# Kernel tuning notes

Hardware: AMD Instinct MI355X
Metric: run time of the kernel (lower is better)

The kernel has to match this reference:

```python
import jax, jax.numpy as jnp
import numpy as np
import math

B, S, E, H = 2, 2048, 768, 12
D = E // H            # head_dim = 64
FFN = 3072            # GeGLU hidden
WIN = 64              # local window size
GLOBAL_IDS = np.array([0])
EPS = 1e-5


def _rope(x):
    # x: [B,H,S,D]; interleaved rotary embedding, theta=10000 (lucidrains RotaryEmbedding)
    d = x.shape[-1]
    s = x.shape[-2]
    inv_freq = 1.0 / (10000.0 ** (jnp.arange(0, d, 2, dtype=jnp.float32) / d))
    freqs = jnp.arange(s, dtype=jnp.float32)[:, None] * inv_freq[None, :]  # [S, D/2]
    freqs = jnp.repeat(freqs, 2, axis=-1)                                   # [S, D]
    cos, sin = jnp.cos(freqs), jnp.sin(freqs)
    xp = x.reshape(x.shape[:-1] + (d // 2, 2))
    x_rot = jnp.stack([-xp[..., 1], xp[..., 0]], axis=-1).reshape(x.shape)
    return x * cos + x_rot * sin


def _layernorm(x, scale, bias):
    mu = jnp.mean(x, axis=-1, keepdims=True)
    var = jnp.mean(jnp.square(x - mu), axis=-1, keepdims=True)
    return (x - mu) * jax.lax.rsqrt(var + EPS) * scale + bias


def setup_inputs() -> dict:
    key = jax.random.key(0)
    ks = jax.random.split(key, 10)
    def xav(k, shape, gain):
        fan_out, fan_in = shape
        std = gain * math.sqrt(2.0 / (fan_in + fan_out))
        return jax.random.normal(k, shape, jnp.float32) * std
    g2 = math.sqrt(2.0)
    g13 = math.sqrt(1.0 / 3.0)
    return {
        "x": jax.random.normal(ks[0], (B, S, E), jnp.float32),
        "rel_pos_bias": jax.random.normal(ks[1], (B, S, S), jnp.float32),
        "mask": jnp.ones((B, S), dtype=bool),
        "wq_w": xav(ks[2], (E, E), g2), "wq_b": jnp.zeros((E,), jnp.float32),
        "wk_w": xav(ks[3], (E, E), g2), "wk_b": jnp.zeros((E,), jnp.float32),
        "wv_w": xav(ks[4], (E, E), g2), "wv_b": jnp.zeros((E,), jnp.float32),
        "fc_w": xav(ks[5], (E, E), g2), "fc_b": jnp.zeros((E,), jnp.float32),
        "pos_coeff": jnp.full((H, 1, 1), 0.01, jnp.float32),
        "gate_w": xav(ks[6], (FFN, E), g13), "gate_b": jnp.zeros((FFN,), jnp.float32),
        "value_w": xav(ks[7], (FFN, E), g2), "value_b": jnp.zeros((FFN,), jnp.float32),
        "down_w": xav(ks[8], (E, FFN), g2), "down_b": jnp.zeros((E,), jnp.float32),
        "ln1_s": jnp.ones((E,), jnp.float32), "ln1_b": jnp.zeros((E,), jnp.float32),
        "ln2_s": jnp.ones((E,), jnp.float32), "ln2_b": jnp.zeros((E,), jnp.float32),
    }


def _sparse_allow(mask):
    # static local-window + global-token pattern, [S,S] bool
    idx = jnp.arange(S)
    allow = jnp.abs(idx[:, None] - idx[None, :]) <= WIN
    gidx = jnp.asarray(GLOBAL_IDS)
    allow = allow.at[gidx, :].set(True)
    allow = allow.at[:, gidx].set(True)
    # combine with padding mask [B,S] broadcast over query rows
    return allow[None, None, :, :] & mask[:, None, None, :]  # [B,1,S,S]


def reference(x, rel_pos_bias, mask, wq_w, wq_b, wk_w, wk_b, wv_w, wv_b,
              fc_w, fc_b, pos_coeff, gate_w, gate_b, value_w, value_b,
              down_w, down_b, ln1_s, ln1_b, ln2_s, ln2_b):
    def heads(t):  # [B,S,E] -> [B,H,S,D]
        return t.reshape(B, S, H, D).transpose(0, 2, 1, 3)

    Q = _rope(heads(x @ wq_w.T + wq_b))
    K = _rope(heads(x @ wk_w.T + wk_b))
    V = heads(x @ wv_w.T + wv_b)

    scores = jnp.einsum('bhqd,bhkd->bhqk', Q, K) / math.sqrt(D)
    scores = scores + pos_coeff[None] * rel_pos_bias[:, None]     # [B,H,S,S]
    allow = _sparse_allow(mask)
    scores = jnp.where(allow, scores, -1e30)
    scores = scores - jnp.max(scores, axis=-1, keepdims=True)
    attn = jax.nn.softmax(scores, axis=-1)
    ctx = jnp.einsum('bhqk,bhkd->bhqd', attn, V)
    ctx = ctx.transpose(0, 2, 1, 3).reshape(B, S, E)
    attn_out = ctx @ fc_w.T + fc_b

    h = _layernorm(x + attn_out, ln1_s, ln1_b)
    gate = jax.nn.gelu(h @ gate_w.T + gate_b, approximate=False)
    ffn = (gate * (h @ value_w.T + value_b)) @ down_w.T + down_b
    return _layernorm(h + ffn, ln2_s, ln2_b)
```

## Files before the change

### kernel.cpp

```cpp
#include <hip/hip_runtime.h>
#include <math.h>

#define B_   2
#define S_   2048
#define E_   768
#define H_   12
#define D_   64
#define FFN_ 3072
#define WIN_ 64
#define MTOT (B_*S_)

typedef unsigned short ushort_t;
typedef unsigned short ushort8 __attribute__((ext_vector_type(8)));
typedef __bf16 bf16x8 __attribute__((ext_vector_type(8)));
typedef float f32x4 __attribute__((ext_vector_type(4)));
typedef _Float16 half_t;

__device__ __forceinline__ float b2f(ushort_t u) {
    union { unsigned int i; float f; } c; c.i = ((unsigned int)u) << 16; return c.f;
}
__device__ __forceinline__ ushort_t f2b(float f) {
    union { float f; unsigned int i; } c; c.f = f;
    unsigned int u = c.i;
    return (ushort_t)((u + 0x7fffu + ((u >> 16) & 1u)) >> 16);
}
__device__ __forceinline__ float gelu_f(float g) {
    return 0.5f * g * (1.f + erff(g * 0.70710678118654752440f));
}

typedef const __attribute__((address_space(1))) void* gptr_t;
typedef __attribute__((address_space(3))) void* lptr_t;
__device__ __forceinline__ void gload16(const void* g, void* l) {
    __builtin_amdgcn_global_load_lds((gptr_t)g,
        (lptr_t)(unsigned int)(unsigned long long)l, 16, 0, 0);
}

__device__ __forceinline__ void cvt8(const float* __restrict__ in,
                                     ushort_t* __restrict__ out, int idx)
{
    const float4* p = (const float4*)(in + (size_t)idx * 8);
    const float4 a = p[0], b = p[1];
    ushort8 o;
    o[0]=f2b(a.x); o[1]=f2b(a.y); o[2]=f2b(a.z); o[3]=f2b(a.w);
    o[4]=f2b(b.x); o[5]=f2b(b.y); o[6]=f2b(b.z); o[7]=f2b(b.w);
    *(ushort8*)(out + (size_t)idx*8) = o;
}

__global__ __launch_bounds__(256)
void prep_fused(const float* __restrict__ x,
                const float* __restrict__ wq_w, const float* __restrict__ wk_w,
                const float* __restrict__ wv_w, const float* __restrict__ fc_w,
                ushort_t* __restrict__ Xb, ushort_t* __restrict__ wqb,
                ushort_t* __restrict__ wkb, ushort_t* __restrict__ wvb,
                ushort_t* __restrict__ fcb, float2* __restrict__ ctab)
{
    const int id = blockIdx.x, tid = threadIdx.x;
    if (id < 1536) {
        cvt8(x, Xb, id*256 + tid);
    } else if (id < 1824) {
        cvt8(wq_w, wqb, (id-1536)*256 + tid);
    } else if (id < 2112) {
        cvt8(wk_w, wkb, (id-1824)*256 + tid);
    } else if (id < 2400) {
        cvt8(wv_w, wvb, (id-2112)*256 + tid);
    } else if (id < 2688) {
        cvt8(fc_w, fcb, (id-2400)*256 + tid);
    } else {
        const int idx = (id-2688)*256 + tid;
        const int s = idx >> 5, i = idx & 31;
        const float inv = exp2f(-(float)i * (13.287712379549449f/32.0f));
        const float fr = (float)s * inv;
        ctab[idx] = make_float2(cosf(fr), sinf(fr));
    }
}

template<int EPI, int BN>
__global__ __launch_bounds__(256)
void gemm_mfma(const ushort_t* __restrict__ A,
               const ushort_t* W0, const float* b0, void* C0,
               const ushort_t* W1, const float* b1, void* C1,
               const ushort_t* W2, const float* b2, void* C2,
               const void* __restrict__ aux, int M, int N, int K)
{
    constexpr int NWC = BN/64, NWR = 4/NWC, WROWS = 128/NWR, MF = WROWS/16;
    const ushort_t* W = W0; const float* bias = b0; void* C = C0;
    if (blockIdx.z == 1) { W = W1; bias = b1; C = C1; }
    else if (blockIdx.z == 2) { W = W2; bias = b2; C = C2; }

    __shared__ __align__(16) ushort_t As[128*32];
    __shared__ __align__(16) ushort_t Bs[BN*32];

    const int tid = threadIdx.x, wv = tid>>6, lane = tid&63;
    const int m0 = blockIdx.y*128, n0 = blockIdx.x*BN;
    const int wr = wv / NWC, wc = wv % NWC;
    const int lr16 = lane & 15, lkb = (lane>>4)<<3;

    f32x4 acc[MF][4];
#pragma unroll
    for (int i=0;i<MF;++i)
#pragma unroll
        for (int j=0;j<4;++j) acc[i][j] = f32x4{0.f,0.f,0.f,0.f};

    const char* Ab = (const char*)(A + (size_t)m0*K);
    const char* Wb = (const char*)(W + (size_t)n0*K);
    const size_t rb = (size_t)K*2;
    const int wbase = wv*1024, lby = lane*16;

    for (int kt = 0; kt < K; kt += 32) {
        const size_t kb = (size_t)kt*2;
        int n_ = wbase + lby;
        gload16(Ab + (size_t)(n_>>6)*rb + kb + (n_&63), (char*)As + wbase);
        n_ += 4096;
        gload16(Ab + (size_t)(n_>>6)*rb + kb + (n_&63), (char*)As + wbase + 4096);
        n_ = wbase + lby;
        gload16(Wb + (size_t)(n_>>6)*rb + kb + (n_&63), (char*)Bs + wbase);
        if (BN == 128) {
            n_ += 4096;
            gload16(Wb + (size_t)(n_>>6)*rb + kb + (n_&63), (char*)Bs + wbase + 4096);
        }
        __syncthreads();
        bf16x8 af[MF], bfr[4];
#pragma unroll
        for (int mf=0; mf<MF; ++mf)
            af[mf] = *(const bf16x8*)&As[(wr*WROWS + mf*16 + lr16)*32 + lkb];
#pragma unroll
        for (int nf=0; nf<4; ++nf)
            bfr[nf] = *(const bf16x8*)&Bs[(wc*64 + nf*16 + lr16)*32 + lkb];
#pragma unroll
        for (int mf=0; mf<MF; ++mf)
#pragma unroll
            for (int nf=0; nf<4; ++nf)
                acc[mf][nf] = __builtin_amdgcn_mfma_f32_16x16x32_bf16(af[mf], bfr[nf], acc[mf][nf], 0,0,0);
        __syncthreads();
    }

    const int colb = n0 + wc*64 + lr16;
    const int rowb = m0 + wr*WROWS + ((lane>>4)<<2);
#pragma unroll
    for (int nf=0; nf<4; ++nf) {
        const int col = colb + nf*16;
        const float bsv = bias[col];
#pragma unroll
        for (int mf=0; mf<MF; ++mf) {
            const int row = rowb + mf*16;
            const f32x4 a = acc[mf][nf];
#pragma unroll
            for (int r=0; r<4; ++r) {
                const size_t off = (size_t)(row+r)*N + col;
                const float v = a[r] + bsv;
                if constexpr (EPI == 0) {
                    ((ushort_t*)C)[off] = f2b(v);
                } else {
                    ((float*)C)[off] = v + ((const float*)aux)[off];
                }
            }
        }
    }
}

__global__ __launch_bounds__(256, 4)
void gemm_qkv(const ushort_t* __restrict__ A,
              const ushort_t* __restrict__ Wqkv,
              const float* __restrict__ bq, const float* __restrict__ bk,
              const float* __restrict__ bv,
              const float2* __restrict__ ctab,
              ushort_t* __restrict__ Qb, ushort_t* __restrict__ Kb,
              ushort_t* __restrict__ Vt)
{
    constexpr int NT   = 24;
    constexpr int ABY  = 128*64;
    constexpr int BUFB = 2*ABY;
    __shared__ __align__(16) char lds[2*BUFB];

    const int id  = blockIdx.x;
    const int xcd = id & 7, w = id >> 3;
    const int gy  = (xcd & 3)*8 + (w & 7);
    const int gx  = (xcd >> 2)*9 + (w >> 3);
    const int m0 = gy*128, n0 = gx*128;

    const int tid = threadIdx.x, wv = tid>>6, l = tid&63;
    const int wr = wv>>1, wc = wv&1;
    const int lr16 = l & 15;
    const int ck = (((l>>4) ^ ((lr16>>1)&3)) << 4);

    const int lr4   = l >> 2;
    const int sslot = ((l & 3) ^ ((l >> 3) & 3)) << 4;
    const char* Agp = (const char*)A    + (size_t)(m0 + wv*32 + lr4)*1536 + sslot;
    const char* Bgp = (const char*)Wqkv + (size_t)(n0 + wv*32 + lr4)*1536 + sslot;

    const int rA0 = (wr*64 +  0 + lr16)*64, rA1 = (wr*64 + 16 + lr16)*64;
    const int rA2 = (wr*64 + 32 + lr16)*64, rA3 = (wr*64 + 48 + lr16)*64;
    const int rB0 = ABY + (wc*64 +  0 + lr16)*64, rB1 = ABY + (wc*64 + 16 + lr16)*64;
    const int rB2 = ABY + (wc*64 + 32 + lr16)*64, rB3 = ABY + (wc*64 + 48 + lr16)*64;

    f32x4 acc[4][4];
#pragma unroll
    for (int i=0;i<4;++i)
#pragma unroll
        for (int j=0;j<4;++j) acc[i][j] = f32x4{0.f,0.f,0.f,0.f};

#define STGQ(tt, cb) { \
    char* dA = lds + (cb)*BUFB + wv*2048; \
    char* dB = lds + (cb)*BUFB + ABY + wv*2048; \
    const size_t ko = (size_t)(tt)*64; \
    gload16(Agp + ko,           dA); \
    gload16(Agp + ko + 16*1536, dA + 1024); \
    gload16(Bgp + ko,           dB); \
    gload16(Bgp + ko + 16*1536, dB + 1024); }

    STGQ(0, 0);
    __syncthreads();

    int c = 0;
#pragma unroll 1
    for (int t = 0; t < NT; ++t) {
        if (t < NT-1) STGQ(t+1, c^1);
        const char* Lb = lds + c*BUFB;
        const bf16x8 a0 = *(const bf16x8*)(Lb + rA0 + ck);
        const bf16x8 a1 = *(const bf16x8*)(Lb + rA1 + ck);
        const bf16x8 a2 = *(const bf16x8*)(Lb + rA2 + ck);
        const bf16x8 a3 = *(const bf16x8*)(Lb + rA3 + ck);
        const bf16x8 b0 = *(const bf16x8*)(Lb + rB0 + ck);
        const bf16x8 b1 = *(const bf16x8*)(Lb + rB1 + ck);
        const bf16x8 b2 = *(const bf16x8*)(Lb + rB2 + ck);
        const bf16x8 b3 = *(const bf16x8*)(Lb + rB3 + ck);
        __builtin_amdgcn_s_setprio(1);
        acc[0][0] = __builtin_amdgcn_mfma_f32_16x16x32_bf16(a0, b0, acc[0][0], 0,0,0);
        acc[1][0] = __builtin_amdgcn_mfma_f32_16x16x32_bf16(a1, b0, acc[1][0], 0,0,0);
        acc[2][0] = __builtin_amdgcn_mfma_f32_16x16x32_bf16(a2, b0, acc[2][0], 0,0,0);
        acc[3][0] = __builtin_amdgcn_mfma_f32_16x16x32_bf16(a3, b0, acc[3][0], 0,0,0);
        acc[0][1] = __builtin_amdgcn_mfma_f32_16x16x32_bf16(a0, b1, acc[0][1], 0,0,0);
        acc[1][1] = __builtin_amdgcn_mfma_f32_16x16x32_bf16(a1, b1, acc[1][1], 0,0,0);
        acc[2][1] = __builtin_amdgcn_mfma_f32_16x16x32_bf16(a2, b1, acc[2][1], 0,0,0);
        acc[3][1] = __builtin_amdgcn_mfma_f32_16x16x32_bf16(a3, b1, acc[3][1], 0,0,0);
        acc[0][2] = __builtin_amdgcn_mfma_f32_16x16x32_bf16(a0, b2, acc[0][2], 0,0,0);
        acc[1][2] = __builtin_amdgcn_mfma_f32_16x16x32_bf16(a1, b2, acc[1][2], 0,0,0);
        acc[2][2] = __builtin_amdgcn_mfma_f32_16x16x32_bf16(a2, b2, acc[2][2], 0,0,0);
        acc[3][2] = __builtin_amdgcn_mfma_f32_16x16x32_bf16(a3, b2, acc[3][2], 0,0,0);
        acc[0][3] = __builtin_amdgcn_mfma_f32_16x16x32_bf16(a0, b3, acc[0][3], 0,0,0);
        acc[1][3] = __builtin_amdgcn_mfma_f32_16x16x32_bf16(a1, b3, acc[1][3], 0,0,0);
        acc[2][3] = __builtin_amdgcn_mfma_f32_16x16x32_bf16(a2, b3, acc[2][3], 0,0,0);
        acc[3][3] = __builtin_amdgcn_mfma_f32_16x16x32_bf16(a3, b3, acc[3][3], 0,0,0);
        __builtin_amdgcn_s_setprio(0);
        __syncthreads();
        c ^= 1;
    }
#undef STGQ

    const int tsel = gx / 6;
    const float* bias = (tsel==0) ? bq : (tsel==1) ? bk : bv;
    ushort_t* out = (tsel==0) ? Qb : Kb;
    const int colb = (gx - tsel*6)*128 + wc*64 + lr16;
    const int rowb = m0 + wr*64 + ((l>>4)<<2);
#pragma unroll
    for (int nf=0; nf<4; ++nf) {
        const int col = colb + nf*16;
        const float bsv = bias[col];
#pragma unroll
        for (int mf=0; mf<4; ++mf) {
            const int row = rowb + mf*16;
            const f32x4 a = acc[mf][nf];
#pragma unroll
            for (int r=0; r<4; ++r) {
                const int rr = row + r;
                const float v = a[r] + bsv;
                if (tsel == 2) {
                    const size_t toff =
                        (((size_t)(rr >> 11)*H_ + (col >> 6))*64 + (col & 63))*(size_t)S_ + (rr & (S_-1));
                    Vt[toff] = f2b(v);
                } else {
                    const int s = rr & (S_-1);
                    const float2 cs = ctab[s*32 + ((col & 63) >> 1)];
                    const float p = __shfl_xor(v, 1);
                    const float rot = (col & 1) ? fmaf(v, cs.x,  p*cs.y)
                                                : fmaf(v, cs.x, -p*cs.y);
                    out[(size_t)rr*E_ + col] = f2b(rot);
                }
            }
        }
    }
}

__global__ __launch_bounds__(256)
void attn_fused(const ushort_t* __restrict__ Qb, const ushort_t* __restrict__ Kb,
                const ushort_t* __restrict__ Vt, const float* __restrict__ rel,
                const float* __restrict__ pos_coeff, ushort_t* __restrict__ ctx,
                const float* __restrict__ gw, const float* __restrict__ vw,
                ushort_t* __restrict__ Wgv)
{
    __shared__ __align__(16) char smem[20480];
    const int bid = blockIdx.x;

    if (bid >= 792) {
        const int idx = (bid - 792)*256 + threadIdx.x;
        const int R   = idx / 96, c8 = idx - R*96;
        const int blk = R >> 6, w = R & 63;
        const float* src = (w < 32 ? gw : vw) + (size_t)(blk*32 + (w & 31))*768 + c8*8;
        const float4 a = ((const float4*)src)[0], b = ((const float4*)src)[1];
        ushort8 o;
        o[0]=f2b(a.x); o[1]=f2b(a.y); o[2]=f2b(a.z); o[3]=f2b(a.w);
        o[4]=f2b(b.x); o[5]=f2b(b.y); o[6]=f2b(b.z); o[7]=f2b(b.w);
        *(ushort8*)(Wgv + (size_t)idx*8) = o;
        return;
    }

    if (bid >= 768) {
// ... 184 lines not shown
    if (q != 0) {
        ushort_t* cb = ctx + ((size_t)(b*S_ + q))*E_ + h*D_;
#pragma unroll
        for (int df = 0; df < 4; ++df)
#pragma unroll
            for (int r = 0; r < 4; ++r)
                cb[df*16 + g*4 + r] = f2b(acc_c[df][r] * inv);
    }
}

__global__ __launch_bounds__(256, 2)
void gemm_geglu(const ushort_t* __restrict__ A,
                const ushort_t* __restrict__ Wgv,
                const float* __restrict__ bgp,
                const float* __restrict__ bvp,
                ushort_t* __restrict__ C,
                const float* __restrict__ down_w,
                ushort_t* __restrict__ downb)
{
    constexpr int NT   = 12;
    constexpr int ABY  = 128*128;
    constexpr int BUFB = 2*ABY;
    __shared__ __align__(16) char lds[2*BUFB];

    const int id  = blockIdx.x;
    if (id >= 1536) {
        cvt8(down_w, downb, (id-1536)*256 + threadIdx.x);
        return;
    }
    const int stI = (id & 7)*3 + ((id >> 3) >> 6);
    const int w64 = (id >> 3) & 63;
    const int gy  = (stI/6)*8 + (w64 >> 3);
    const int gx  = (stI%6)*8 + (w64 & 7);
    const int m0 = gy*128, n0 = gx*128;

    const int tid = threadIdx.x, wv = tid>>6, l = tid&63;
    const int wr = wv>>1, wc = wv&1;
    const int lr16 = l & 15, g16b = (l>>4)<<4;
    const int xr = (lr16 & 7) << 4;

    const int lrow = l >> 3;
    const int swzc = ((l & 7) ^ lrow) << 4;
    const char* Agp = (const char*)A   + (size_t)(m0 + wv*32 + lrow)*1536 + swzc;
    const char* Bgp = (const char*)Wgv + (size_t)(n0 + wv*32 + lrow)*1536 + swzc;

    const int rA0 = (wr*64 +  0 + lr16)*128, rA1 = (wr*64 + 16 + lr16)*128;
    const int rA2 = (wr*64 + 32 + lr16)*128, rA3 = (wr*64 + 48 + lr16)*128;
    const int rB0 = ABY + (wc*64 +  0 + lr16)*128, rB1 = ABY + (wc*64 + 16 + lr16)*128;
    const int rB2 = ABY + (wc*64 + 32 + lr16)*128, rB3 = ABY + (wc*64 + 48 + lr16)*128;
    const int ck0 = g16b ^ xr, ck1 = (64 + g16b) ^ xr;

    f32x4 acc[4][4];
#pragma unroll
    for (int i=0;i<4;++i)
#pragma unroll
        for (int j=0;j<4;++j) acc[i][j] = f32x4{0.f,0.f,0.f,0.f};

#define STG(tt, cb) { \
    char* dA = lds + (cb)*BUFB + wv*4096; \
    char* dB = lds + (cb)*BUFB + ABY + wv*4096; \
    const size_t ko = (size_t)(tt)*128; \
    gload16(Agp + ko,           dA); \
    gload16(Agp + ko +  8*1536, dA + 1024); \
    gload16(Agp + ko + 16*1536, dA + 2048); \
    gload16(Agp + ko + 24*1536, dA + 3072); \
    gload16(Bgp + ko,           dB); \
    gload16(Bgp + ko +  8*1536, dB + 1024); \
    gload16(Bgp + ko + 16*1536, dB + 2048); \
    gload16(Bgp + ko + 24*1536, dB + 3072); }

    STG(0, 0);
    __syncthreads();

    int c = 0;
#pragma unroll 1
    for (int t = 0; t < NT; ++t) {
        if (t < NT-1) STG(t+1, c^1);
        const char* Lb = lds + c*BUFB;
        const bf16x8 a0 = *(const bf16x8*)(Lb + rA0 + ck0);
        const bf16x8 a1 = *(const bf16x8*)(Lb + rA1 + ck0);
        const bf16x8 a2 = *(const bf16x8*)(Lb + rA2 + ck0);
        const bf16x8 a3 = *(const bf16x8*)(Lb + rA3 + ck0);
        const bf16x8 b0 = *(const bf16x8*)(Lb + rB0 + ck0);
        const bf16x8 b1 = *(const bf16x8*)(Lb + rB1 + ck0);
        const bf16x8 b2 = *(const bf16x8*)(Lb + rB2 + ck0);
        const bf16x8 b3 = *(const bf16x8*)(Lb + rB3 + ck0);
        const bf16x8 e0 = *(const bf16x8*)(Lb + rA0 + ck1);
        const bf16x8 e1 = *(const bf16x8*)(Lb + rA1 + ck1);
        const bf16x8 e2 = *(const bf16x8*)(Lb + rA2 + ck1);
        const bf16x8 e3 = *(const bf16x8*)(Lb + rA3 + ck1);
        const bf16x8 f0 = *(const bf16x8*)(Lb + rB0 + ck1);
        const bf16x8 f1 = *(const bf16x8*)(Lb + rB1 + ck1);
        const bf16x8 f2 = *(const bf16x8*)(Lb + rB2 + ck1);
        const bf16x8 f3 = *(const bf16x8*)(Lb + rB3 + ck1);
        __builtin_amdgcn_s_setprio(1);
        acc[0][0] = __builtin_amdgcn_mfma_f32_16x16x32_bf16(a0, b0, acc[0][0], 0,0,0);
        acc[1][0] = __builtin_amdgcn_mfma_f32_16x16x32_bf16(a1, b0, acc[1][0], 0,0,0);
        acc[2][0] = __builtin_amdgcn_mfma_f32_16x16x32_bf16(a2, b0, acc[2][0], 0,0,0);
        acc[3][0] = __builtin_amdgcn_mfma_f32_16x16x32_bf16(a3, b0, acc[3][0], 0,0,0);
        acc[0][1] = __builtin_amdgcn_mfma_f32_16x16x32_bf16(a0, b1, acc[0][1], 0,0,0);
        acc[1][1] = __builtin_amdgcn_mfma_f32_16x16x32_bf16(a1, b1, acc[1][1], 0,0,0);
        acc[2][1] = __builtin_amdgcn_mfma_f32_16x16x32_bf16(a2, b1, acc[2][1], 0,0,0);
        acc[3][1] = __builtin_amdgcn_mfma_f32_16x16x32_bf16(a3, b1, acc[3][1], 0,0,0);
        acc[0][2] = __builtin_amdgcn_mfma_f32_16x16x32_bf16(a0, b2, acc[0][2], 0,0,0);
        acc[1][2] = __builtin_amdgcn_mfma_f32_16x16x32_bf16(a1, b2, acc[1][2], 0,0,0);
        acc[2][2] = __builtin_amdgcn_mfma_f32_16x16x32_bf16(a2, b2, acc[2][2], 0,0,0);
        acc[3][2] = __builtin_amdgcn_mfma_f32_16x16x32_bf16(a3, b2, acc[3][2], 0,0,0);
        acc[0][3] = __builtin_amdgcn_mfma_f32_16x16x32_bf16(a0, b3, acc[0][3], 0,0,0);
        acc[1][3] = __builtin_amdgcn_mfma_f32_16x16x32_bf16(a1, b3, acc[1][3], 0,0,0);
        acc[2][3] = __builtin_amdgcn_mfma_f32_16x16x32_bf16(a2, b3, acc[2][3], 0,0,0);
        acc[3][3] = __builtin_amdgcn_mfma_f32_16x16x32_bf16(a3, b3, acc[3][3], 0,0,0);
        acc[0][0] = __builtin_amdgcn_mfma_f32_16x16x32_bf16(e0, f0, acc[0][0], 0,0,0);
        acc[1][0] = __builtin_amdgcn_mfma_f32_16x16x32_bf16(e1, f0, acc[1][0], 0,0,0);
        acc[2][0] = __builtin_amdgcn_mfma_f32_16x16x32_bf16(e2, f0, acc[2][0], 0,0,0);
        acc[3][0] = __builtin_amdgcn_mfma_f32_16x16x32_bf16(e3, f0, acc[3][0], 0,0,0);
        acc[0][1] = __builtin_amdgcn_mfma_f32_16x16x32_bf16(e0, f1, acc[0][1], 0,0,0);
        acc[1][1] = __builtin_amdgcn_mfma_f32_16x16x32_bf16(e1, f1, acc[1][1], 0,0,0);
        acc[2][1] = __builtin_amdgcn_mfma_f32_16x16x32_bf16(e2, f1, acc[2][1], 0,0,0);
        acc[3][1] = __builtin_amdgcn_mfma_f32_16x16x32_bf16(e3, f1, acc[3][1], 0,0,0);
        acc[0][2] = __builtin_amdgcn_mfma_f32_16x16x32_bf16(e0, f2, acc[0][2], 0,0,0);
        acc[1][2] = __builtin_amdgcn_mfma_f32_16x16x32_bf16(e1, f2, acc[1][2], 0,0,0);
        acc[2][2] = __builtin_amdgcn_mfma_f32_16x16x32_bf16(e2, f2, acc[2][2], 0,0,0);
        acc[3][2] = __builtin_amdgcn_mfma_f32_16x16x32_bf16(e3, f2, acc[3][2], 0,0,0);
        acc[0][3] = __builtin_amdgcn_mfma_f32_16x16x32_bf16(e0, f3, acc[0][3], 0,0,0);
        acc[1][3] = __builtin_amdgcn_mfma_f32_16x16x32_bf16(e1, f3, acc[1][3], 0,0,0);
        acc[2][3] = __builtin_amdgcn_mfma_f32_16x16x32_bf16(e2, f3, acc[2][3], 0,0,0);
        acc[3][3] = __builtin_amdgcn_mfma_f32_16x16x32_bf16(e3, f3, acc[3][3], 0,0,0);
        __builtin_amdgcn_s_setprio(0);
        __syncthreads();
        c ^= 1;
    }
#undef STG

    const int colb = gx*64 + wc*32 + lr16;
    const int rowb = m0 + wr*64 + ((l>>4)<<2);
#pragma unroll
    for (int nf=0; nf<2; ++nf) {
        const int col = colb + nf*16;
        const float bgv = bgp[col], bvv = bvp[col];
#pragma unroll
        for (int mf=0; mf<4; ++mf) {
            const int row = rowb + mf*16;
            const f32x4 gq = acc[mf][nf];
            const f32x4 vq = acc[mf][nf+2];
#pragma unroll
            for (int r=0; r<4; ++r) {
                C[(size_t)(row+r)*3072 + col] =
                    f2b(gelu_f(gq[r] + bgv) * (vq[r] + bvv));
            }
        }
    }
}

__global__ __launch_bounds__(256, 3)
void gemm_down(const ushort_t* __restrict__ A,
               const ushort_t* __restrict__ Wd,
               const float* __restrict__ bias,
               float* __restrict__ P0,
               half_t* __restrict__ P1)
{
    constexpr int NT   = 24;
    constexpr int ABY  = 128*128;
    constexpr int BBY  = 64*128;
    constexpr int BUFB = ABY + BBY;
    __shared__ __align__(16) char lds[2*BUFB];

    const int id   = blockIdx.x;
    const int work = (id & 7)*96 + (id >> 3);
    const int z    = work / 384;
    const int r    = work - z*384;
    const int gy   = r / 12, gx = r - gy*12;
    const int m0 = gy*128, n0 = gx*64;

    const int tid = threadIdx.x, wv = tid>>6, l = tid&63;
    const int wr = wv>>1, wc = wv&1;
    const int lr16 = l & 15, g16b = (l>>4)<<4;
    const int xr = (lr16 & 7) << 4;

    const int lrow = l >> 3;
    const int swzc = ((l & 7) ^ lrow) << 4;
    const size_t kbase = (size_t)z*3072;
    const char* Agp = (const char*)A  + (size_t)(m0 + wv*32 + lrow)*6144 + kbase + swzc;
    const char* Bgp = (const char*)Wd + (size_t)(n0 + wv*16 + lrow)*6144 + kbase + swzc;

    const int rA0 = (wr*64 +  0 + lr16)*128, rA1 = (wr*64 + 16 + lr16)*128;
    const int rA2 = (wr*64 + 32 + lr16)*128, rA3 = (wr*64 + 48 + lr16)*128;
    const int rB0 = ABY + (wc*32 +  0 + lr16)*128;
    const int rB1 = ABY + (wc*32 + 16 + lr16)*128;
    const int ck0 = g16b ^ xr, ck1 = (64 + g16b) ^ xr;

    f32x4 acc[4][2];
#pragma unroll
    for (int i=0;i<4;++i)
#pragma unroll
        for (int j=0;j<2;++j) acc[i][j] = f32x4{0.f,0.f,0.f,0.f};

#define STGD(tt, cb) { \
    char* dA = lds + (cb)*BUFB + wv*4096; \
    char* dB = lds + (cb)*BUFB + ABY + wv*2048; \
    const size_t ko = (size_t)(tt)*128; \
    gload16(Agp + ko,           dA); \
    gload16(Agp + ko +  8*6144, dA + 1024); \
    gload16(Agp + ko + 16*6144, dA + 2048); \
    gload16(Agp + ko + 24*6144, dA + 3072); \
    gload16(Bgp + ko,           dB); \
    gload16(Bgp + ko +  8*6144, dB + 1024); }

    STGD(0, 0);
    __syncthreads();

    int c = 0;
#pragma unroll 1
    for (int t = 0; t < NT; ++t) {
        if (t < NT-1) STGD(t+1, c^1);
        const char* Lb = lds + c*BUFB;
        const bf16x8 a0 = *(const bf16x8*)(Lb + rA0 + ck0);
        const bf16x8 a1 = *(const bf16x8*)(Lb + rA1 + ck0);
        const bf16x8 a2 = *(const bf16x8*)(Lb + rA2 + ck0);
        const bf16x8 a3 = *(const bf16x8*)(Lb + rA3 + ck0);
        const bf16x8 b0 = *(const bf16x8*)(Lb + rB0 + ck0);
        const bf16x8 b1 = *(const bf16x8*)(Lb + rB1 + ck0);
        const bf16x8 e0 = *(const bf16x8*)(Lb + rA0 + ck1);
        const bf16x8 e1 = *(const bf16x8*)(Lb + rA1 + ck1);
        const bf16x8 e2 = *(const bf16x8*)(Lb + rA2 + ck1);
        const bf16x8 e3 = *(const bf16x8*)(Lb + rA3 + ck1);
        const bf16x8 f0 = *(const bf16x8*)(Lb + rB0 + ck1);
        const bf16x8 f1 = *(const bf16x8*)(Lb + rB1 + ck1);
        __builtin_amdgcn_s_setprio(1);
        acc[0][0] = __builtin_amdgcn_mfma_f32_16x16x32_bf16(a0, b0, acc[0][0], 0,0,0);
        acc[1][0] = __builtin_amdgcn_mfma_f32_16x16x32_bf16(a1, b0, acc[1][0], 0,0,0);
        acc[2][0] = __builtin_amdgcn_mfma_f32_16x16x32_bf16(a2, b0, acc[2][0], 0,0,0);
        acc[3][0] = __builtin_amdgcn_mfma_f32_16x16x32_bf16(a3, b0, acc[3][0], 0,0,0);
        acc[0][1] = __builtin_amdgcn_mfma_f32_16x16x32_bf16(a0, b1, acc[0][1], 0,0,0);
        acc[1][1] = __builtin_amdgcn_mfma_f32_16x16x32_bf16(a1, b1, acc[1][1], 0,0,0);
        acc[2][1] = __builtin_amdgcn_mfma_f32_16x16x32_bf16(a2, b1, acc[2][1], 0,0,0);
        acc[3][1] = __builtin_amdgcn_mfma_f32_16x16x32_bf16(a3, b1, acc[3][1], 0,0,0);
        acc[0][0] = __builtin_amdgcn_mfma_f32_16x16x32_bf16(e0, f0, acc[0][0], 0,0,0);
        acc[1][0] = __builtin_amdgcn_mfma_f32_16x16x32_bf16(e1, f0, acc[1][0], 0,0,0);
        acc[2][0] = __builtin_amdgcn_mfma_f32_16x16x32_bf16(e2, f0, acc[2][0], 0,0,0);
        acc[3][0] = __builtin_amdgcn_mfma_f32_16x16x32_bf16(e3, f0, acc[3][0], 0,0,0);
        acc[0][1] = __builtin_amdgcn_mfma_f32_16x16x32_bf16(e0, f1, acc[0][1], 0,0,0);
        acc[1][1] = __builtin_amdgcn_mfma_f32_16x16x32_bf16(e1, f1, acc[1][1], 0,0,0);
        acc[2][1] = __builtin_amdgcn_mfma_f32_16x16x32_bf16(e2, f1, acc[2][1], 0,0,0);
        acc[3][1] = __builtin_amdgcn_mfma_f32_16x16x32_bf16(e3, f1, acc[3][1], 0,0,0);
        __builtin_amdgcn_s_setprio(0);
        __syncthreads();
        c ^= 1;
    }
#undef STGD

    const int colb = n0 + wc*32 + lr16;
    const int rowb = m0 + wr*64 + ((l>>4)<<2);
#pragma unroll
    for (int nf=0; nf<2; ++nf) {
        const int col = colb + nf*16;
        const float bsv = bias[col];
#pragma unroll
        for (int mf=0; mf<4; ++mf) {
            const int row = rowb + mf*16;
            const f32x4 a = acc[mf][nf];
#pragma unroll
            for (int rr=0; rr<4; ++rr) {
                const size_t off = (size_t)(row+rr)*E_ + col;
                if (z == 0) P0[off] = a[rr] + bsv;
                else        P1[off] = (half_t)a[rr];
            }
        }
    }
}

template<bool WB>
__global__ __launch_bounds__(256)
void ln_kernel(const float* __restrict__ in, const float* __restrict__ gam,
               const float* __restrict__ bet, float* __restrict__ out,
               ushort_t* __restrict__ outb)
{
    const int row = blockIdx.x;
    const float* r = in + (size_t)row * E_;
    const int tid = threadIdx.x;
    const float v0 = r[tid], v1 = r[tid+256], v2 = r[tid+512];
    float s  = v0+v1+v2;
    float ss = v0*v0+v1*v1+v2*v2;
#pragma unroll
    for (int off = 32; off > 0; off >>= 1) {
        s  += __shfl_xor(s, off);
        ss += __shfl_xor(ss, off);
    }
    __shared__ float rs[4], rss[4];
    const int wv = tid >> 6, lane = tid & 63;
    if (lane == 0) { rs[wv] = s; rss[wv] = ss; }
    __syncthreads();
    s  = rs[0]+rs[1]+rs[2]+rs[3];
    ss = rss[0]+rss[1]+rss[2]+rss[3];
    const float mu  = s * (1.f/E_);
    const float var = ss * (1.f/E_) - mu*mu;
    const float rstd = rsqrtf(var + 1e-5f);
    float* o = out + (size_t)row * E_;
    const float o0 = (v0-mu)*rstd*gam[tid    ] + bet[tid    ];
    const float o1 = (v1-mu)*rstd*gam[tid+256] + bet[tid+256];
    const float o2 = (v2-mu)*rstd*gam[tid+512] + bet[tid+512];
    o[tid] = o0; o[tid+256] = o1; o[tid+512] = o2;
    if constexpr (WB) {
        ushort_t* ob = outb + (size_t)row * E_;
        ob[tid] = f2b(o0); ob[tid+256] = f2b(o1); ob[tid+512] = f2b(o2);
    }
}

__global__ __launch_bounds__(256)
void ln3_kernel(const float* __restrict__ p0, const half_t* __restrict__ p1,
                const float* __restrict__ res, const float* __restrict__ gam,
                const float* __restrict__ bet, float* __restrict__ out)
{
    const int row = blockIdx.x;
    const size_t base = (size_t)row * E_;
    const int tid = threadIdx.x;
    const float v0 = p0[base+tid]     + (float)p1[base+tid]     + res[base+tid];
    const float v1 = p0[base+tid+256] + (float)p1[base+tid+256] + res[base+tid+256];
    const float v2 = p0[base+tid+512] + (float)p1[base+tid+512] + res[base+tid+512];
    float s  = v0+v1+v2;
    float ss = v0*v0+v1*v1+v2*v2;
#pragma unroll
    for (int off = 32; off > 0; off >>= 1) {
        s  += __shfl_xor(s, off);
        ss += __shfl_xor(ss, off);
    }
    __shared__ float rs[4], rss[4];
    const int wv = tid >> 6, lane = tid & 63;
    if (lane == 0) { rs[wv] = s; rss[wv] = ss; }
    __syncthreads();
    s  = rs[0]+rs[1]+rs[2]+rs[3];
    ss = rss[0]+rss[1]+rss[2]+rss[3];
    const float mu  = s * (1.f/E_);
    const float var = ss * (1.f/E_) - mu*mu;
    const float rstd = rsqrtf(var + 1e-5f);
    float* o = out + base;
    o[tid]     = (v0-mu)*rstd*gam[tid    ] + bet[tid    ];
    o[tid+256] = (v1-mu)*rstd*gam[tid+256] + bet[tid+256];
    o[tid+512] = (v2-mu)*rstd*gam[tid+512] + bet[tid+512];
}

extern "C" void kernel_launch(void* const* d_in, const int* in_sizes, int n_in,
                              void* d_out, int out_size, void* d_ws, size_t ws_size,
                              hipStream_t stream)
{
    const float* x      = (const float*)d_in[0];
    const float* rel    = (const float*)d_in[1];
    const float* wq_w   = (const float*)d_in[3];
    const float* wq_b   = (const float*)d_in[4];
    const float* wk_w   = (const float*)d_in[5];
    const float* wk_b   = (const float*)d_in[6];
    const float* wv_w   = (const float*)d_in[7];
    const float* wv_b   = (const float*)d_in[8];
    const float* fc_w   = (const float*)d_in[9];
    const float* fc_b   = (const float*)d_in[10];
    const float* pos_c  = (const float*)d_in[11];
    const float* gate_w = (const float*)d_in[12];
    const float* gate_b = (const float*)d_in[13];
    const float* value_w= (const float*)d_in[14];
    const float* value_b= (const float*)d_in[15];
    const float* down_w = (const float*)d_in[16];
    const float* down_b = (const float*)d_in[17];
    const float* ln1_s  = (const float*)d_in[18];
    const float* ln1_b  = (const float*)d_in[19];
    const float* ln2_s  = (const float*)d_in[20];
    const float* ln2_b  = (const float*)d_in[21];
    float* out = (float*)d_out;

    char* W = (char*)d_ws;
    ushort_t* Qb     = (ushort_t*)(W + 0);
    ushort_t* Kb     = (ushort_t*)(W + 6291456);
    ushort_t* Vt     = (ushort_t*)(W + 12582912);
    ushort_t* Cxb    = (ushort_t*)(W + 18874368);
    ushort_t* GpB    = (ushort_t*)(W + 0);
    ushort_t* Xb     = (ushort_t*)(W + 25165824);
    ushort_t* wqb    = (ushort_t*)(W + 31457280);
    ushort_t* wkb    = (ushort_t*)(W + 32636928);
    ushort_t* wvb    = (ushort_t*)(W + 33816576);
    ushort_t* fcb    = (ushort_t*)(W + 34996224);
    ushort_t* Wgv    = (ushort_t*)(W + 25165824);
    ushort_t* downb  = (ushort_t*)(W + 34996224);
    float*    AO     = (float*)   (W + 39714816);
    float*    Hb     = (float*)   (W + 52297728);
    ushort_t* Hbb    = (ushort_t*)(W + 64880640);
    half_t*   P1h    = (half_t*)  (W + 64880640);
    float2*   ctab   = (float2*)  (W + 71172096);

    prep_fused<<<2944, 256, 0, stream>>>(x, wq_w, wk_w, wv_w, fc_w,
                                         Xb, wqb, wkb, wvb, fcb, ctab);

    gemm_qkv<<<576, 256, 0, stream>>>(Xb, wqb, wq_b, wk_b, wv_b, ctab, Qb, Kb, Vt);

    attn_fused<<<3096, 256, 0, stream>>>(Qb, Kb, Vt, rel, pos_c, Cxb,
                                         gate_w, value_w, Wgv);

    gemm_mfma<1,64><<<dim3(E_/64, MTOT/128, 1), 256, 0, stream>>>(
        Cxb, fcb, fc_b, AO, nullptr, nullptr, nullptr, nullptr, nullptr, nullptr,
        x, MTOT, E_, E_);

    ln_kernel<true><<<MTOT, 256, 0, stream>>>(AO, ln1_s, ln1_b, Hb, Hbb);

    gemm_geglu<<<dim3(2688), 256, 0, stream>>>(Hbb, Wgv, gate_b, value_b, GpB,
                                               down_w, downb);

    gemm_down<<<dim3(768), 256, 0, stream>>>(GpB, downb, down_b, AO, P1h);

    ln3_kernel<<<MTOT, 256, 0, stream>>>(AO, P1h, Hb, ln2_s, ln2_b, out);
}
```

Before: 217.2 us.

## Replace fc GEMM with split-K pipelined kernel and unify with down projection

The simple single-buffered fc projection GEMM is replaced by a templated split-K kernel with double-buffered, swizzled LDS staging, 128x128 tiles and two K halves. One half writes fp32 with bias and residual, the other writes fp16 partials. The layernorm now sums both partials. The down projection reuses the same template with 128x128 tiles instead of 128x64, which halves its grid to 384 blocks. The fp16 partial adds rounding error, and fewer blocks may lower occupancy.

```diff
diff --git a/kernel.cpp b/kernel.cpp
--- a/kernel.cpp
+++ b/kernel.cpp
@@ -74,84 +74,146 @@
     }
 }
 
-template<int EPI, int BN>
-__global__ __launch_bounds__(256)
-void gemm_mfma(const ushort_t* __restrict__ A,
-               const ushort_t* W0, const float* b0, void* C0,
-               const ushort_t* W1, const float* b1, void* C1,
-               const ushort_t* W2, const float* b2, void* C2,
-               const void* __restrict__ aux, int M, int N, int K)
+template<int KTOT, bool RESID>
+__global__ __launch_bounds__(256, 2)
+void gemm_splitk(const ushort_t* __restrict__ A,
+                 const ushort_t* __restrict__ Wd,
+                 const float* __restrict__ bias,
+                 const float* __restrict__ res,
+                 float* __restrict__ P0,
+                 half_t* __restrict__ P1)
 {
-    constexpr int NWC = BN/64, NWR = 4/NWC, WROWS = 128/NWR, MF = WROWS/16;
-    const ushort_t* W = W0; const float* bias = b0; void* C = C0;
-    if (blockIdx.z == 1) { W = W1; bias = b1; C = C1; }
-    else if (blockIdx.z == 2) { W = W2; bias = b2; C = C2; }
-
-    __shared__ __align__(16) ushort_t As[128*32];
-    __shared__ __align__(16) ushort_t Bs[BN*32];
-
-    const int tid = threadIdx.x, wv = tid>>6, lane = tid&63;
-    const int m0 = blockIdx.y*128, n0 = blockIdx.x*BN;
-    const int wr = wv / NWC, wc = wv % NWC;
-    const int lr16 = lane & 15, lkb = (lane>>4)<<3;
-
-    f32x4 acc[MF][4];
-#pragma unroll
-    for (int i=0;i<MF;++i)
+    constexpr int NT   = KTOT/128;
+    constexpr int ABY  = 128*128;
+    constexpr int BUFB = 2*ABY;
+    __shared__ __align__(16) char lds[2*BUFB];
+
+    const int id   = blockIdx.x;
+    const int work = (id & 7)*48 + (id >> 3);
+    const int z    = work / 192;
+    const int r    = work - z*192;
+    const int gy   = r / 6, gx = r - gy*6;
+    const int m0 = gy*128, n0 = gx*128;
+
+    const int tid = threadIdx.x, wv = tid>>6, l = tid&63;
+    const int wr = wv>>1, wc = wv&1;
+    const int lr16 = l & 15, g16b = (l>>4)<<4;
+    const int xr = (lr16 & 7) << 4;
+
+    const int lrow = l >> 3;
+    const int swzc = ((l & 7) ^ lrow) << 4;
+    constexpr size_t RB = (size_t)KTOT*2;
+    const size_t kbase = (size_t)z*KTOT;
+    const char* Agp = (const char*)A  + (size_t)(m0 + wv*32 + lrow)*RB + kbase + swzc;
+    const char* Bgp = (const char*)Wd + (size_t)(n0 + wv*32 + lrow)*RB + kbase + swzc;
+
+    const int rA0 = (wr*64 +  0 + lr16)*128, rA1 = (wr*64 + 16 + lr16)*128;
+    const int rA2 = (wr*64 + 32 + lr16)*128, rA3 = (wr*64 + 48 + lr16)*128;
+    const int rB0 = ABY + (wc*64 +  0 + lr16)*128, rB1 = ABY + (wc*64 + 16 + lr16)*128;
+    const int rB2 = ABY + (wc*64 + 32 + lr16)*128, rB3 = ABY + (wc*64 + 48 + lr16)*128;
+    const int ck0 = g16b ^ xr, ck1 = (64 + g16b) ^ xr;
+
+    f32x4 acc[4][4];
+#pragma unroll
+    for (int i=0;i<4;++i)
 #pragma unroll
         for (int j=0;j<4;++j) acc[i][j] = f32x4{0.f,0.f,0.f,0.f};
 
-    const char* Ab = (const char*)(A + (size_t)m0*K);
-    const char* Wb = (const char*)(W + (size_t)n0*K);
-    const size_t rb = (size_t)K*2;
-    const int wbase = wv*1024, lby = lane*16;
-
-    for (int kt = 0; kt < K; kt += 32) {
-        const size_t kb = (size_t)kt*2;
-        int n_ = wbase + lby;
-        gload16(Ab + (size_t)(n_>>6)*rb + kb + (n_&63), (char*)As + wbase);
-        n_ += 4096;
-        gload16(Ab + (size_t)(n_>>6)*rb + kb + (n_&63), (char*)As + wbase + 4096);
-        n_ = wbase + lby;
-        gload16(Wb + (size_t)(n_>>6)*rb + kb + (n_&63), (char*)Bs + wbase);
-        if (BN == 128) {
-            n_ += 4096;
-            gload16(Wb + (size_t)(n_>>6)*rb + kb + (n_&63), (char*)Bs + wbase + 4096);
-        }
+#define STGS(tt, cb) { \
+    char* dA = lds + (cb)*BUFB + wv*4096; \
+    char* dB = lds + (cb)*BUFB + ABY + wv*4096; \
+    const size_t ko = (size_t)(tt)*128; \
+    gload16(Agp + ko,         dA); \
+    gload16(Agp + ko +  8*RB, dA + 1024); \
+    gload16(Agp + ko + 16*RB, dA + 2048); \
+    gload16(Agp + ko + 24*RB, dA + 3072); \
+    gload16(Bgp + ko,         dB); \
+    gload16(Bgp + ko +  8*RB, dB + 1024); \
+    gload16(Bgp + ko + 16*RB, dB + 2048); \
+    gload16(Bgp + ko + 24*RB, dB + 3072); }
+
+    STGS(0, 0);
+    __syncthreads();
+
+    int c = 0;
+#pragma unroll 1
+    for (int t = 0; t < NT; ++t) {
+        if (t < NT-1) STGS(t+1, c^1);
+        const char* Lb = lds + c*BUFB;
+        const bf16x8 a0 = *(const bf16x8*)(Lb + rA0 + ck0);
+        const bf16x8 a1 = *(const bf16x8*)(Lb + rA1 + ck0);
+        const bf16x8 a2 = *(const bf16x8*)(Lb + rA2 + ck0);
+        const bf16x8 a3 = *(const bf16x8*)(Lb + rA3 + ck0);
+        const bf16x8 b0 = *(const bf16x8*)(Lb + rB0 + ck0);
+        const bf16x8 b1 = *(const bf16x8*)(Lb + rB1 + ck0);
+        const bf16x8 b2 = *(const bf16x8*)(Lb + rB2 + ck0);
+        const bf16x8 b3 = *(const bf16x8*)(Lb + rB3 + ck0);
+        const bf16x8 e0 = *(const bf16x8*)(Lb + rA0 + ck1);
+        const bf16x8 e1 = *(const bf16x8*)(Lb + rA1 + ck1);
+        const bf16x8 e2 = *(const bf16x8*)(Lb + rA2 + ck1);
+        const bf16x8 e3 = *(const bf16x8*)(Lb + rA3 + ck1);
+        const bf16x8 f0 = *(const bf16x8*)(Lb + rB0 + ck1);
+        const bf16x8 f1 = *(const bf16x8*)(Lb + rB1 + ck1);
+        const bf16x8 f2 = *(const bf16x8*)(Lb + rB2 + ck1);
+        const bf16x8 f3 = *(const bf16x8*)(Lb + rB3 + ck1);
+        __builtin_amdgcn_s_setprio(1);
+        acc[0][0] = __builtin_amdgcn_mfma_f32_16x16x32_bf16(a0, b0, acc[0][0], 0,0,0);
+        acc[1][0] = __builtin_amdgcn_mfma_f32_16x16x32_bf16(a1, b0, acc[1][0], 0,0,0);
+        acc[2][0] = __builtin_amdgcn_mfma_f32_16x16x32_bf16(a2, b0, acc[2][0], 0,0,0);
+        acc[3][0] = __builtin_amdgcn_mfma_f32_16x16x32_bf16(a3, b0, acc[3][0], 0,0,0);
+        acc[0][1] = __builtin_amdgcn_mfma_f32_16x16x32_bf16(a0, b1, acc[0][1], 0,0,0);
+        acc[1][1] = __builtin_amdgcn_mfma_f32_16x16x32_bf16(a1, b1, acc[1][1], 0,0,0);
+        acc[2][1] = __builtin_amdgcn_mfma_f32_16x16x32_bf16(a2, b1, acc[2][1], 0,0,0);
+        acc[3][1] = __builtin_amdgcn_mfma_f32_16x16x32_bf16(a3, b1, acc[3][1], 0,0,0);
+        acc[0][2] = __builtin_amdgcn_mfma_f32_16x16x32_bf16(a0, b2, acc[0][2], 0,0,0);
+        acc[1][2] = __builtin_amdgcn_mfma_f32_16x16x32_bf16(a1, b2, acc[1][2], 0,0,0);
+        acc[2][2] = __builtin_amdgcn_mfma_f32_16x16x32_bf16(a2, b2, acc[2][2], 0,0,0);
+        acc[3][2] = __builtin_amdgcn_mfma_f32_16x16x32_bf16(a3, b2, acc[3][2], 0,0,0);
+        acc[0][3] = __builtin_amdgcn_mfma_f32_16x16x32_bf16(a0, b3, acc[0][3], 0,0,0);
+        acc[1][3] = __builtin_amdgcn_mfma_f32_16x16x32_bf16(a1, b3, acc[1][3], 0,0,0);
+        acc[2][3] = __builtin_amdgcn_mfma_f32_16x16x32_bf16(a2, b3, acc[2][3], 0,0,0);
+        acc[3][3] = __builtin_amdgcn_mfma_f32_16x16x32_bf16(a3, b3, acc[3][3], 0,0,0);
+        acc[0][0] = __builtin_amdgcn_mfma_f32_16x16x32_bf16(e0, f0, acc[0][0], 0,0,0);
+        acc[1][0] = __builtin_amdgcn_mfma_f32_16x16x32_bf16(e1, f0, acc[1][0], 0,0,0);
+        acc[2][0] = __builtin_amdgcn_mfma_f32_16x16x32_bf16(e2, f0, acc[2][0], 0,0,0);
+        acc[3][0] = __builtin_amdgcn_mfma_f32_16x16x32_bf16(e3, f0, acc[3][0], 0,0,0);
+        acc[0][1] = __builtin_amdgcn_mfma_f32_16x16x32_bf16(e0, f1, acc[0][1], 0,0,0);
+        acc[1][1] = __builtin_amdgcn_mfma_f32_16x16x32_bf16(e1, f1, acc[1][1], 0,0,0);
+        acc[2][1] = __builtin_amdgcn_mfma_f32_16x16x32_bf16(e2, f1, acc[2][1], 0,0,0);
+        acc[3][1] = __builtin_amdgcn_mfma_f32_16x16x32_bf16(e3, f1, acc[3][1], 0,0,0);
+        acc[0][2] = __builtin_amdgcn_mfma_f32_16x16x32_bf16(e0, f2, acc[0][2], 0,0,0);
+        acc[1][2] = __builtin_amdgcn_mfma_f32_16x16x32_bf16(e1, f2, acc[1][2], 0,0,0);
+        acc[2][2] = __builtin_amdgcn_mfma_f32_16x16x32_bf16(e2, f2, acc[2][2], 0,0,0);
+        acc[3][2] = __builtin_amdgcn_mfma_f32_16x16x32_bf16(e3, f2, acc[3][2], 0,0,0);
+        acc[0][3] = __builtin_amdgcn_mfma_f32_16x16x32_bf16(e0, f3, acc[0][3], 0,0,0);
+        acc[1][3] = __builtin_amdgcn_mfma_f32_16x16x32_bf16(e1, f3, acc[1][3], 0,0,0);
+        acc[2][3] = __builtin_amdgcn_mfma_f32_16x16x32_bf16(e2, f3, acc[2][3], 0,0,0);
+        acc[3][3] = __builtin_amdgcn_mfma_f32_16x16x32_bf16(e3, f3, acc[3][3], 0,0,0);
+        __builtin_amdgcn_s_setprio(0);
         __syncthreads();
-        bf16x8 af[MF], bfr[4];
-#pragma unroll
-        for (int mf=0; mf<MF; ++mf)
-            af[mf] = *(const bf16x8*)&As[(wr*WROWS + mf*16 + lr16)*32 + lkb];
-#pragma unroll
-        for (int nf=0; nf<4; ++nf)
-            bfr[nf] = *(const bf16x8*)&Bs[(wc*64 + nf*16 + lr16)*32 + lkb];
-#pragma unroll
-        for (int mf=0; mf<MF; ++mf)
-#pragma unroll
-            for (int nf=0; nf<4; ++nf)
-                acc[mf][nf] = __builtin_amdgcn_mfma_f32_16x16x32_bf16(af[mf], bfr[nf], acc[mf][nf], 0,0,0);
-        __syncthreads();
-    }
+        c ^= 1;
+    }
+#undef STGS
 
     const int colb = n0 + wc*64 + lr16;
-    const int rowb = m0 + wr*WROWS + ((lane>>4)<<2);
+    const int rowb = m0 + wr*64 + ((l>>4)<<2);
 #pragma unroll
     for (int nf=0; nf<4; ++nf) {
         const int col = colb + nf*16;
         const float bsv = bias[col];
 #pragma unroll
-        for (int mf=0; mf<MF; ++mf) {
+        for (int mf=0; mf<4; ++mf) {
             const int row = rowb + mf*16;
             const f32x4 a = acc[mf][nf];
 #pragma unroll
-            for (int r=0; r<4; ++r) {
-                const size_t off = (size_t)(row+r)*N + col;
-                const float v = a[r] + bsv;
-                if constexpr (EPI == 0) {
-                    ((ushort_t*)C)[off] = f2b(v);
+            for (int rr=0; rr<4; ++rr) {
+                const size_t off = (size_t)(row+rr)*E_ + col;
+                if (z == 0) {
+                    float v = a[rr] + bsv;
+                    if constexpr (RESID) v += res[off];
+                    P0[off] = v;
                 } else {
-                    ((float*)C)[off] = v + ((const float*)aux)[off];
+                    P1[off] = (half_t)a[rr];
                 }
             }
         }
@@ -642,133 +704,17 @@
     }
 }
 
-__global__ __launch_bounds__(256, 3)
-void gemm_down(const ushort_t* __restrict__ A,
-               const ushort_t* __restrict__ Wd,
-               const float* __restrict__ bias,
-               float* __restrict__ P0,
-               half_t* __restrict__ P1)
-{
-    constexpr int NT   = 24;
-    constexpr int ABY  = 128*128;
-    constexpr int BBY  = 64*128;
-    constexpr int BUFB = ABY + BBY;
-    __shared__ __align__(16) char lds[2*BUFB];
-
-    const int id   = blockIdx.x;
-    const int work = (id & 7)*96 + (id >> 3);
-    const int z    = work / 384;
-    const int r    = work - z*384;
-    const int gy   = r / 12, gx = r - gy*12;
-    const int m0 = gy*128, n0 = gx*64;
-
-    const int tid = threadIdx.x, wv = tid>>6, l = tid&63;
-    const int wr = wv>>1, wc = wv&1;
-    const int lr16 = l & 15, g16b = (l>>4)<<4;
-    const int xr = (lr16 & 7) << 4;
-
-    const int lrow = l >> 3;
-    const int swzc = ((l & 7) ^ lrow) << 4;
-    const size_t kbase = (size_t)z*3072;
-    const char* Agp = (const char*)A  + (size_t)(m0 + wv*32 + lrow)*6144 + kbase + swzc;
-    const char* Bgp = (const char*)Wd + (size_t)(n0 + wv*16 + lrow)*6144 + kbase + swzc;
-
-    const int rA0 = (wr*64 +  0 + lr16)*128, rA1 = (wr*64 + 16 + lr16)*128;
-    const int rA2 = (wr*64 + 32 + lr16)*128, rA3 = (wr*64 + 48 + lr16)*128;
-    const int rB0 = ABY + (wc*32 +  0 + lr16)*128;
-    const int rB1 = ABY + (wc*32 + 16 + lr16)*128;
-    const int ck0 = g16b ^ xr, ck1 = (64 + g16b) ^ xr;
-
-    f32x4 acc[4][2];
-#pragma unroll
-    for (int i=0;i<4;++i)
-#pragma unroll
-        for (int j=0;j<2;++j) acc[i][j] = f32x4{0.f,0.f,0.f,0.f};
-
-#define STGD(tt, cb) { \
-    char* dA = lds + (cb)*BUFB + wv*4096; \
-    char* dB = lds + (cb)*BUFB + ABY + wv*2048; \
-    const size_t ko = (size_t)(tt)*128; \
-    gload16(Agp + ko,           dA); \
-    gload16(Agp + ko +  8*6144, dA + 1024); \
-    gload16(Agp + ko + 16*6144, dA + 2048); \
-    gload16(Agp + ko + 24*6144, dA + 3072); \
-    gload16(Bgp + ko,           dB); \
-    gload16(Bgp + ko +  8*6144, dB + 1024); }
-
-    STGD(0, 0);
-    __syncthreads();
-
-    int c = 0;
-#pragma unroll 1
-    for (int t = 0; t < NT; ++t) {
-        if (t < NT-1) STGD(t+1, c^1);
-        const char* Lb = lds + c*BUFB;
-        const bf16x8 a0 = *(const bf16x8*)(Lb + rA0 + ck0);
-        const bf16x8 a1 = *(const bf16x8*)(Lb + rA1 + ck0);
-        const bf16x8 a2 = *(const bf16x8*)(Lb + rA2 + ck0);
-        const bf16x8 a3 = *(const bf16x8*)(Lb + rA3 + ck0);
-        const bf16x8 b0 = *(const bf16x8*)(Lb + rB0 + ck0);
-        const bf16x8 b1 = *(const bf16x8*)(Lb + rB1 + ck0);
-        const bf16x8 e0 = *(const bf16x8*)(Lb + rA0 + ck1);
-        const bf16x8 e1 = *(const bf16x8*)(Lb + rA1 + ck1);
-        const bf16x8 e2 = *(const bf16x8*)(Lb + rA2 + ck1);
-        const bf16x8 e3 = *(const bf16x8*)(Lb + rA3 + ck1);
-        const bf16x8 f0 = *(const bf16x8*)(Lb + rB0 + ck1);
-        const bf16x8 f1 = *(const bf16x8*)(Lb + rB1 + ck1);
-        __builtin_amdgcn_s_setprio(1);
-        acc[0][0] = __builtin_amdgcn_mfma_f32_16x16x32_bf16(a0, b0, acc[0][0], 0,0,0);
-        acc[1][0] = __builtin_amdgcn_mfma_f32_16x16x32_bf16(a1, b0, acc[1][0], 0,0,0);
-        acc[2][0] = __builtin_amdgcn_mfma_f32_16x16x32_bf16(a2, b0, acc[2][0], 0,0,0);
-        acc[3][0] = __builtin_amdgcn_mfma_f32_16x16x32_bf16(a3, b0, acc[3][0], 0,0,0);
-        acc[0][1] = __builtin_amdgcn_mfma_f32_16x16x32_bf16(a0, b1, acc[0][1], 0,0,0);
-        acc[1][1] = __builtin_amdgcn_mfma_f32_16x16x32_bf16(a1, b1, acc[1][1], 0,0,0);
-        acc[2][1] = __builtin_amdgcn_mfma_f32_16x16x32_bf16(a2, b1, acc[2][1], 0,0,0);
-        acc[3][1] = __builtin_amdgcn_mfma_f32_16x16x32_bf16(a3, b1, acc[3][1], 0,0,0);
-        acc[0][0] = __builtin_amdgcn_mfma_f32_16x16x32_bf16(e0, f0, acc[0][0], 0,0,0);
-        acc[1][0] = __builtin_amdgcn_mfma_f32_16x16x32_bf16(e1, f0, acc[1][0], 0,0,0);
-        acc[2][0] = __builtin_amdgcn_mfma_f32_16x16x32_bf16(e2, f0, acc[2][0], 0,0,0);
-        acc[3][0] = __builtin_amdgcn_mfma_f32_16x16x32_bf16(e3, f0, acc[3][0], 0,0,0);
-        acc[0][1] = __builtin_amdgcn_mfma_f32_16x16x32_bf16(e0, f1, acc[0][1], 0,0,0);
-        acc[1][1] = __builtin_amdgcn_mfma_f32_16x16x32_bf16(e1, f1, acc[1][1], 0,0,0);
-        acc[2][1] = __builtin_amdgcn_mfma_f32_16x16x32_bf16(e2, f1, acc[2][1], 0,0,0);
-        acc[3][1] = __builtin_amdgcn_mfma_f32_16x16x32_bf16(e3, f1, acc[3][1], 0,0,0);
-        __builtin_amdgcn_s_setprio(0);
-        __syncthreads();
-        c ^= 1;
-    }
-#undef STGD
-
-    const int colb = n0 + wc*32 + lr16;
-    const int rowb = m0 + wr*64 + ((l>>4)<<2);
-#pragma unroll
-    for (int nf=0; nf<2; ++nf) {
-        const int col = colb + nf*16;
-        const float bsv = bias[col];
-#pragma unroll
-        for (int mf=0; mf<4; ++mf) {
-            const int row = rowb + mf*16;
-            const f32x4 a = acc[mf][nf];
-#pragma unroll
-            for (int rr=0; rr<4; ++rr) {
-                const size_t off = (size_t)(row+rr)*E_ + col;
-                if (z == 0) P0[off] = a[rr] + bsv;
-                else        P1[off] = (half_t)a[rr];
-            }
-        }
-    }
-}
-
-template<bool WB>
 __global__ __launch_bounds__(256)
-void ln_kernel(const float* __restrict__ in, const float* __restrict__ gam,
-               const float* __restrict__ bet, float* __restrict__ out,
-               ushort_t* __restrict__ outb)
+void ln1_fused(const float* __restrict__ p0, const half_t* __restrict__ p1,
+               const float* __restrict__ gam, const float* __restrict__ bet,
+               float* __restrict__ out, ushort_t* __restrict__ outb)
 {
     const int row = blockIdx.x;
-    const float* r = in + (size_t)row * E_;
+    const size_t base = (size_t)row * E_;
     const int tid = threadIdx.x;
-    const float v0 = r[tid], v1 = r[tid+256], v2 = r[tid+512];
+    const float v0 = p0[base+tid]     + (float)p1[base+tid];
+    const float v1 = p0[base+tid+256] + (float)p1[base+tid+256];
+    const float v2 = p0[base+tid+512] + (float)p1[base+tid+512];
     float s  = v0+v1+v2;
     float ss = v0*v0+v1*v1+v2*v2;
 #pragma unroll
@@ -785,15 +731,13 @@
     const float mu  = s * (1.f/E_);
     const float var = ss * (1.f/E_) - mu*mu;
     const float rstd = rsqrtf(var + 1e-5f);
-    float* o = out + (size_t)row * E_;
+    float* o = out + base;
+    ushort_t* ob = outb + base;
     const float o0 = (v0-mu)*rstd*gam[tid    ] + bet[tid    ];
     const float o1 = (v1-mu)*rstd*gam[tid+256] + bet[tid+256];
     const float o2 = (v2-mu)*rstd*gam[tid+512] + bet[tid+512];
     o[tid] = o0; o[tid+256] = o1; o[tid+512] = o2;
-    if constexpr (WB) {
-        ushort_t* ob = outb + (size_t)row * E_;
-        ob[tid] = f2b(o0); ob[tid+256] = f2b(o1); ob[tid+512] = f2b(o2);
-    }
+    ob[tid] = f2b(o0); ob[tid+256] = f2b(o1); ob[tid+512] = f2b(o2);
 }
 
 __global__ __launch_bounds__(256)
@@ -861,6 +805,7 @@
     ushort_t* Kb     = (ushort_t*)(W + 6291456);
     ushort_t* Vt     = (ushort_t*)(W + 12582912);
     ushort_t* Cxb    = (ushort_t*)(W + 18874368);
+    half_t*   P1fc   = (half_t*)  (W + 0);
     ushort_t* GpB    = (ushort_t*)(W + 0);
     ushort_t* Xb     = (ushort_t*)(W + 25165824);
     ushort_t* wqb    = (ushort_t*)(W + 31457280);
@@ -883,16 +828,16 @@
     attn_fused<<<3096, 256, 0, stream>>>(Qb, Kb, Vt, rel, pos_c, Cxb,
                                          gate_w, value_w, Wgv);
 
-    gemm_mfma<1,64><<<dim3(E_/64, MTOT/128, 1), 256, 0, stream>>>(
-        Cxb, fcb, fc_b, AO, nullptr, nullptr, nullptr, nullptr, nullptr, nullptr,
-        x, MTOT, E_, E_);
-
-    ln_kernel<true><<<MTOT, 256, 0, stream>>>(AO, ln1_s, ln1_b, Hb, Hbb);
+    gemm_splitk<768, true><<<384, 256, 0, stream>>>(
+        Cxb, fcb, fc_b, x, AO, P1fc);
+
+    ln1_fused<<<MTOT, 256, 0, stream>>>(AO, P1fc, ln1_s, ln1_b, Hb, Hbb);
 
     gemm_geglu<<<dim3(2688), 256, 0, stream>>>(Hbb, Wgv, gate_b, value_b, GpB,
                                                down_w, downb);
 
-    gemm_down<<<dim3(768), 256, 0, stream>>>(GpB, downb, down_b, AO, P1h);
+    gemm_splitk<3072, false><<<384, 256, 0, stream>>>(
+        GpB, downb, down_b, nullptr, AO, P1h);
 
     ln3_kernel<<<MTOT, 256, 0, stream>>>(AO, P1h, Hb, ln2_s, ln2_b, out);
 }
```

Measured after the change: 220.5 us. About the same (+1.5%).
